# Performance work log

Measured on AMD Instinct MI355X. Metric: run time of the kernel, lower is better.

Reference implementation:

```python
import jax, jax.numpy as jnp
import numpy as np

B, S, D_IN, D_OUT, H = 4, 2048, 1024, 1024, 16
HD = D_OUT // H


def setup_inputs() -> dict:
    key = jax.random.key(0)
    ks = jax.random.split(key, 6)
    s_in = 1.0 / np.sqrt(D_IN)
    s_out = 1.0 / np.sqrt(D_OUT)
    return {
        "x": jax.random.normal(ks[0], (B, S, D_IN), dtype=jnp.float32),
        "W_q": jax.random.uniform(ks[1], (D_OUT, D_IN), jnp.float32, -s_in, s_in),
        "W_k": jax.random.uniform(ks[2], (D_OUT, D_IN), jnp.float32, -s_in, s_in),
        "W_v": jax.random.uniform(ks[3], (D_OUT, D_IN), jnp.float32, -s_in, s_in),
        "W_o": jax.random.uniform(ks[4], (D_OUT, D_OUT), jnp.float32, -s_out, s_out),
        "b_o": jax.random.uniform(ks[5], (D_OUT,), jnp.float32, -s_out, s_out),
    }


def reference(x, W_q, W_k, W_v, W_o, b_o):
    b, s, _ = x.shape
    # torch Linear: y = x @ W.T  (no qkv bias)
    q = (x @ W_q.T).reshape(b, s, H, HD).transpose(0, 2, 1, 3)  # [b,h,s,hd]
    k = (x @ W_k.T).reshape(b, s, H, HD).transpose(0, 2, 1, 3)
    v = (x @ W_v.T).reshape(b, s, H, HD).transpose(0, 2, 1, 3)
    scores = jnp.einsum("bhqd,bhkd->bhqk", q, k)  # [b,h,s,s]
    causal = jnp.triu(jnp.ones((s, s), dtype=bool), k=1)
    scores = jnp.where(causal, -jnp.inf, scores)
    attn = jax.nn.softmax(scores / np.sqrt(HD), axis=-1)
    # dropout p=0.0 -> identity
    ctx = jnp.einsum("bhqk,bhkd->bhqd", attn, v)  # [b,h,s,hd]
    ctx = ctx.transpose(0, 2, 1, 3).reshape(b, s, D_OUT)
    return ctx @ W_o.T + b_o
```

## Files before the change

kernel.cpp:

```cpp
#include <hip/hip_runtime.h>
#include <cstdint>
#include <cstddef>

#define S_LEN  2048
#define NHEAD  16
#define HDIM   64
#define KD     1024
#define BSROWS 8192

typedef __attribute__((ext_vector_type(4))) float          floatx4;
typedef __attribute__((ext_vector_type(8))) __bf16         bf16x8;
typedef __attribute__((ext_vector_type(8))) unsigned short ushort8v;
typedef __attribute__((ext_vector_type(4))) unsigned short ushort4v;
typedef __attribute__((ext_vector_type(4))) float          float4v;

__device__ __forceinline__ unsigned short f2bf(float f) {
  unsigned int u = __float_as_uint(f);
  u += 0x7fffu + ((u >> 16) & 1u);
  return (unsigned short)(u >> 16);
}

#if __has_builtin(__builtin_amdgcn_exp2f)
#define EXP2F(x) __builtin_amdgcn_exp2f(x)
#else
#define EXP2F(x) exp2f(x)
#endif

__device__ __forceinline__ unsigned int pack2bf(float a, float b) {
#if __has_builtin(__builtin_amdgcn_perm)
  return __builtin_amdgcn_perm(__float_as_uint(b), __float_as_uint(a), 0x07060302);
#else
  return (__float_as_uint(a) >> 16) | (__float_as_uint(b) & 0xffff0000u);
#endif
}

__device__ __forceinline__ void async_cp16(const void* gsrc, void* ldst) {
  __builtin_amdgcn_global_load_lds(
      (__attribute__((address_space(1))) void*)gsrc,
      (__attribute__((address_space(3))) void*)ldst,
      16, 0, 0);
}

#define XN4 2097152
#define WN4 262144

__global__ __launch_bounds__(256) void cvt_kernel(
    const float* __restrict__ x,  const float* __restrict__ wq,
    const float* __restrict__ wk, const float* __restrict__ wv,
    const float* __restrict__ wo,
    unsigned short* __restrict__ xb, unsigned short* __restrict__ wqkvb,
    unsigned short* __restrict__ wob)
{
  const int i = blockIdx.x * 256 + threadIdx.x;
  const float* src; unsigned short* dst; int off;
  if (i < XN4) { src = x; dst = xb; off = i; }
  else {
    const int j = i - XN4;
    if (j < WN4)          { src = wq; dst = wqkvb;           off = j; }
    else if (j < 2*WN4)   { src = wk; dst = wqkvb + 4*WN4;   off = j - WN4; }
    else if (j < 3*WN4)   { src = wv; dst = wqkvb + 8*WN4;   off = j - 2*WN4; }
    else                  { src = wo; dst = wob;             off = j - 3*WN4; }
  }
  const float4v v = ((const float4v*)src)[off];
  ushort4v o;
  o.x = f2bf(v.x); o.y = f2bf(v.y); o.z = f2bf(v.z); o.w = f2bf(v.w);
  ((ushort4v*)dst)[off] = o;
}

template<bool SWAP>
__device__ __forceinline__ void kloop128(
    const unsigned short* __restrict__ gA,
    const unsigned short* __restrict__ gB,
    unsigned short* smem, floatx4 (&acc)[4][4],
    const int wave, const int quad, const int l15,
    const int wr, const int wc)
{
  {
    unsigned short* lA = smem + wave * 1024;
    unsigned short* lB = smem + 4096 + wave * 1024;
    async_cp16(gA,                    lA);
    async_cp16(gA + (size_t)16 * KD,  lA + 512);
    async_cp16(gB,                    lB);
    async_cp16(gB + (size_t)16 * KD,  lB + 512);
  }
  const int lsw = (l15 >> 1) & 3;

#pragma unroll 2
  for (int it = 0; it < 32; it++) {
    asm volatile("s_waitcnt vmcnt(0) lgkmcnt(0)\n\ts_barrier" ::: "memory");
    if (it + 1 < 32) {
      const int nb = (it + 1) & 1;
      const int ko = (it + 1) * 32;
      unsigned short* lA = smem + nb * 8192 + wave * 1024;
      unsigned short* lB = smem + nb * 8192 + 4096 + wave * 1024;
      async_cp16(gA + ko,                   lA);
      async_cp16(gA + ko + (size_t)16 * KD, lA + 512);
      async_cp16(gB + ko,                   lB);
      async_cp16(gB + ko + (size_t)16 * KD, lB + 512);
    }
    const unsigned short* As = smem + (it & 1) * 8192;
    const unsigned short* Bs = As + 4096;

    bf16x8 af[4], bfrag[4];
#pragma unroll
    for (int i = 0; i < 4; i++)
      af[i] = *(const bf16x8*)&As[(wr * 64 + i * 16 + l15) * 32 + (quad ^ lsw) * 8];
#pragma unroll
    for (int j = 0; j < 4; j++)
      bfrag[j] = *(const bf16x8*)&Bs[(wc * 64 + j * 16 + l15) * 32 + (quad ^ lsw) * 8];
#pragma unroll
    for (int i = 0; i < 4; i++)
#pragma unroll
      for (int j = 0; j < 4; j++) {
        if (SWAP)
          acc[i][j] = __builtin_amdgcn_mfma_f32_16x16x32_bf16(bfrag[j], af[i], acc[i][j], 0, 0, 0);
        else
          acc[i][j] = __builtin_amdgcn_mfma_f32_16x16x32_bf16(af[i], bfrag[j], acc[i][j], 0, 0, 0);
      }
  }
}

__global__ __launch_bounds__(256) void gemm_qkv(
    const unsigned short* __restrict__ A,
    const unsigned short* __restrict__ Bw,
    unsigned short* __restrict__ Qo,
    unsigned short* __restrict__ Ko,
    unsigned short* __restrict__ Vto)
{
  __shared__ unsigned short smem[17408];
  const int tid  = threadIdx.x;
  const int wave = tid >> 6, lane = tid & 63;
  const int quad = lane >> 4, l15 = lane & 15;
  const int wr = wave >> 1, wc = wave & 1;
  const int m0 = blockIdx.x * 128, n0 = blockIdx.y * 128;

  const int srow = lane >> 2;
  const int scol = ((lane & 3) ^ ((srow >> 1) & 3)) * 8;
  const unsigned short* gA = A  + (size_t)(m0 + wave * 32 + srow) * KD + scol;
  const unsigned short* gB = Bw + (size_t)(n0 + wave * 32 + srow) * KD + scol;

  const floatx4 fzero = {0.f, 0.f, 0.f, 0.f};
  floatx4 acc[4][4];
#pragma unroll
  for (int i = 0; i < 4; i++)
#pragma unroll
    for (int j = 0; j < 4; j++) acc[i][j] = fzero;

  const int which = n0 >> 10;
  const int h0 = (n0 & 1023) >> 6;
  const int b = m0 >> 11, sl = m0 & 2047;

  if (which < 2) {
    kloop128<true>(gA, gB, smem, acc, wave, quad, l15, wr, wc);
    unsigned short* dst = which ? Ko : Qo;
    const float scale = which ? 1.0f : 0.18033688011112042f;
    __syncthreads();
    const int srw = wr * 64 + l15;
    const int scl = wc * 64 + quad * 4;
#pragma unroll
    for (int i = 0; i < 4; i++)
#pragma unroll
      for (int j = 0; j < 4; j++) {
        ushort4v t4;
#pragma unroll
        for (int r = 0; r < 4; r++) t4[r] = f2bf(acc[i][j][r] * scale);
        *(ushort4v*)&smem[(srw + i * 16) * 136 + scl + j * 16] = t4;
      }
    __syncthreads();
#pragma unroll
    for (int t = 0; t < 8; t++) {
      const int c   = t * 256 + tid;
      const int hd8 = (c & 7) * 8;
      const int hh  = (c >> 3) & 1;
      const int s   = c >> 4;
      const ushort8v val = *(const ushort8v*)&smem[s * 136 + hh * 64 + hd8];
      *(ushort8v*)&dst[((size_t)((b * NHEAD + h0 + hh) * S_LEN + sl + s)) * HDIM + hd8] = val;
    }
  } else {
    kloop128<false>(gA, gB, smem, acc, wave, quad, l15, wr, wc);
    __syncthreads();
    const int crow = wr * 64 + quad * 4;
    const int ccol = wc * 64 + l15;
#pragma unroll
    for (int i = 0; i < 4; i++)
#pragma unroll
      for (int j = 0; j < 4; j++) {
        ushort4v t4;
#pragma unroll
        for (int r = 0; r < 4; r++) t4[r] = f2bf(acc[i][j][r]);
        *(ushort4v*)&smem[(ccol + j * 16) * 136 + crow + i * 16] = t4;
      }
    __syncthreads();
#pragma unroll
    for (int t = 0; t < 8; t++) {
      const int c  = t * 256 + tid;
      const int nl = c >> 4, sc = (c & 15) * 8;
      const ushort8v val = *(const ushort8v*)&smem[nl * 136 + sc];
      *(ushort8v*)&Vto[((size_t)((b * NHEAD + h0 + (nl >> 6)) * HDIM + (nl & 63))) * S_LEN + sl + sc] = val;
    }
  }
}

__global__ __launch_bounds__(512, 6) void attn_kernel(
    const unsigned short* __restrict__ Qg_,
    const unsigned short* __restrict__ Kg_,
    const unsigned short* __restrict__ Vtg_,
    unsigned short* __restrict__ CTX)
{
  __shared__ unsigned short smem[25088];
  const int tid  = threadIdx.x, wave = tid >> 6, lane = tid & 63;
  const int quad = lane >> 4, l15 = lane & 15;
  unsigned short* Pw = smem + 16384 + wave * 1088;

  const int bh = (int)blockIdx.x;
  const int yy = (int)blockIdx.y;
  const int qt = (yy < 4) ? yy : (yy < 8) ? (11 - yy) : (yy < 12) ? yy : (27 - yy);
  const int q0 = qt * 128;
  const size_t base = (size_t)bh * (S_LEN * HDIM);
  const unsigned short* Qg  = Qg_  + base;
  const unsigned short* Kg  = Kg_  + base;
  const unsigned short* Vtg = Vtg_ + base;
  const int qw = q0 + wave * 16;

  const int strow = lane >> 3;
  const int stxc  = (lane & 7) ^ strow;
  const unsigned short* kstage = Kg  + (size_t)(wave * 8 + strow) * HDIM  + stxc * 8;
  const unsigned short* vstage = Vtg + (size_t)(wave * 8 + strow) * S_LEN + stxc * 8;
  unsigned short* kd0 = smem + wave * 512;
  unsigned short* vd0 = smem + 4096 + wave * 512;

  async_cp16(kstage, kd0);
  async_cp16(vstage, vd0);

  bf16x8 qf[2];
#pragma unroll
  for (int ks = 0; ks < 2; ks++)
    qf[ks] = *(const bf16x8*)&Qg[(size_t)(qw + l15) * HDIM + ks * 32 + quad * 8];

  const int sw0 = ((quad)     ^ (l15 & 7)) * 8;
  const int sw1 = ((4 + quad) ^ (l15 & 7)) * 8;

  const floatx4 fzero = {0.f, 0.f, 0.f, 0.f};
  floatx4 O[4];
  float l_part = 0.f;
#pragma unroll
  for (int mt = 0; mt < 4; mt++) O[mt] = fzero;

  const int ntiles = 2 * qt + 2;

  for (int j = 0; j < ntiles; j++) {
    asm volatile("s_waitcnt vmcnt(0) lgkmcnt(0)\n\ts_barrier" ::: "memory");
    if (j + 1 < ntiles) {
      const int nb = (j + 1) & 1;
      async_cp16(kstage + (size_t)(j + 1) * 64 * HDIM, kd0 + nb * 8192);
      async_cp16(vstage + (size_t)(j + 1) * 64,        vd0 + nb * 8192);
    }
    const int k0 = j * 64;
    if (k0 > qw + 15) continue;
    const unsigned short* Ksb = smem + (j & 1) * 8192;
    const unsigned short* Vsb = Ksb + 4096;
    const int krel = qw + 15 - k0;

    floatx4 sa[4];
#pragma unroll
    for (int kt = 0; kt < 4; kt++) sa[kt] = fzero;
    __builtin_amdgcn_s_setprio(1);
#pragma unroll
    for (int kt = 0; kt < 4; kt++) {
      if (kt * 16 <= krel) {
        const unsigned short* kr = &Ksb[(kt * 16 + l15) * 64];
        sa[kt] = __builtin_amdgcn_mfma_f32_16x16x32_bf16(*(const bf16x8*)(kr + sw0), qf[0], sa[kt], 0, 0, 0);
        sa[kt] = __builtin_amdgcn_mfma_f32_16x16x32_bf16(*(const bf16x8*)(kr + sw1), qf[1], sa[kt], 0, 0, 0);
      }
    }
    __builtin_amdgcn_s_setprio(0);

    const int qrow = qw + l15;
#pragma unroll
    for (int kt = 0; kt < 4; kt++) {
      const int kbase = k0 + kt * 16;
      unsigned short* pdst = &Pw[l15 * 68 + kt * 16 + quad * 4];
      if (kt * 16 <= krel) {
        if (kbase + 15 > qw) {
#pragma unroll
          for (int r = 0; r < 4; r++)
            if (kbase + quad * 4 + r > qrow) sa[kt][r] = -INFINITY;
        }
        const float p0 = EXP2F(sa[kt][0]), p1 = EXP2F(sa[kt][1]);
        const float p2 = EXP2F(sa[kt][2]), p3 = EXP2F(sa[kt][3]);
        l_part += (p0 + p1) + (p2 + p3);
        uint2 pk; pk.x = pack2bf(p0, p1); pk.y = pack2bf(p2, p3);
        *(uint2*)pdst = pk;
      } else if ((kt >> 1) * 32 <= krel) {
        uint2 z; z.x = 0u; z.y = 0u;
        *(uint2*)pdst = z;
      }
    }
    asm volatile("s_waitcnt lgkmcnt(0)" ::: "memory");

#pragma unroll
    for (int ks = 0; ks < 2; ks++) {
      if (ks * 32 > krel) break;
      const unsigned short* ps = &Pw[l15 * 68 + ks * 32 + quad * 8];
      union { ushort4v h[2]; bf16x8 v; } pu;
      pu.h[0] = *(const ushort4v*)ps;
      pu.h[1] = *(const ushort4v*)(ps + 4);
      __builtin_amdgcn_s_setprio(1);
#pragma unroll
      for (int mt = 0; mt < 4; mt++) {
        const bf16x8 vf = *(const bf16x8*)(&Vsb[(mt * 16 + l15) * 64] + (ks ? sw1 : sw0));
        O[mt] = __builtin_amdgcn_mfma_f32_16x16x32_bf16(vf, pu.v, O[mt], 0, 0, 0);
      }
      __builtin_amdgcn_s_setprio(0);
    }
  }

#pragma unroll
  for (int d = 16; d < 64; d <<= 1)
    l_part += __shfl_xor(l_part, d, 64);

  {
    const float inv = 1.0f / l_part;
#pragma unroll
    for (int mt = 0; mt < 4; mt++)
#pragma unroll
      for (int a = 0; a < 2; a++) {
        const unsigned int pk =
            (unsigned int)f2bf(O[mt][2 * a] * inv) |
            ((unsigned int)f2bf(O[mt][2 * a + 1] * inv) << 16);
        *(unsigned int*)&Pw[l15 * 68 + mt * 16 + quad * 4 + 2 * a] = pk;
      }
  }
  asm volatile("s_waitcnt lgkmcnt(0)" ::: "memory");
  const int b = bh >> 4, h = bh & 15;
#pragma unroll
  for (int it = 0; it < 2; it++) {
    const int g = it * 64 + lane;
    const int row = g >> 3, c8 = (g & 7) * 8;
    union { ushort4v h[2]; ushort8v v; } ou;
    ou.h[0] = *(const ushort4v*)&Pw[row * 68 + c8];
    ou.h[1] = *(const ushort4v*)&Pw[row * 68 + c8 + 4];
    const int s = qw + row;
    *(ushort8v*)&CTX[((size_t)(b * S_LEN + s)) * KD + h * HDIM + c8] = ou.v;
  }
}

__global__ __launch_bounds__(256) void gemm_out(
    const unsigned short* __restrict__ A,
    const unsigned short* __restrict__ Bw,
    const float* __restrict__ bias,
    float* __restrict__ out)
{
  __shared__ unsigned short smem[16384];
  const int tid  = threadIdx.x;
  const int wave = tid >> 6, lane = tid & 63;
  const int quad = lane >> 4, l15 = lane & 15;
  const int wr = wave >> 1, wc = wave & 1;
  const int m0 = blockIdx.x * 128, n0 = blockIdx.y * 128;

  const int srow = lane >> 2;
  const int scol = ((lane & 3) ^ ((srow >> 1) & 3)) * 8;
  const unsigned short* gA = A  + (size_t)(m0 + wave * 32 + srow) * KD + scol;
  const unsigned short* gB = Bw + (size_t)(n0 + wave * 32 + srow) * KD + scol;

  const floatx4 fzero = {0.f, 0.f, 0.f, 0.f};
  floatx4 acc[4][4];
#pragma unroll
  for (int i = 0; i < 4; i++)
#pragma unroll
    for (int j = 0; j < 4; j++) acc[i][j] = fzero;

  kloop128<true>(gA, gB, smem, acc, wave, quad, l15, wr, wc);

#pragma unroll
  for (int j = 0; j < 4; j++) {
    const int nb4 = n0 + wc * 64 + j * 16 + quad * 4;
    const float4v bb = *(const float4v*)&bias[nb4];
#pragma unroll
    for (int i = 0; i < 4; i++) {
      const int m = m0 + wr * 64 + i * 16 + l15;
      float4v st;
#pragma unroll
      for (int r = 0; r < 4; r++) st[r] = acc[i][j][r] + bb[r];
      *(float4v*)&out[(size_t)m * KD + nb4] = st;
    }
  }
}

extern "C" void kernel_launch(void* const* d_in, const int* in_sizes, int n_in,
                              void* d_out, int out_size, void* d_ws, size_t ws_size,
                              hipStream_t stream) {
  (void)in_sizes; (void)n_in; (void)out_size;
  const float* x  = (const float*)d_in[0];
  const float* wq = (const float*)d_in[1];
  const float* wk = (const float*)d_in[2];
  const float* wv = (const float*)d_in[3];
  const float* wo = (const float*)d_in[4];
  const float* bo = (const float*)d_in[5];
  float* out = (float*)d_out;

  if (ws_size < (size_t)92274688) return;
  char* ws = (char*)d_ws;
  unsigned short* xb    = (unsigned short*)(ws);
  unsigned short* wqkvb = (unsigned short*)(ws + (size_t)16777216);
  unsigned short* wob   = (unsigned short*)(ws + (size_t)23068672);
  unsigned short* qws   = (unsigned short*)(ws + (size_t)25165824);
  unsigned short* kws   = (unsigned short*)(ws + (size_t)41943040);
  unsigned short* vtws  = (unsigned short*)(ws + (size_t)58720256);
  unsigned short* ctxws = (unsigned short*)(ws + (size_t)75497472);

  cvt_kernel<<<12288, 256, 0, stream>>>(x, wq, wk, wv, wo, xb, wqkvb, wob);
  gemm_qkv<<<dim3(64, 24), 256, 0, stream>>>(xb, wqkvb, qws, kws, vtws);
  attn_kernel<<<dim3(64, 16), 512, 0, stream>>>(qws, kws, vtws, ctxws);
  gemm_out<<<dim3(64, 8), 256, 0, stream>>>(ctxws, wob, bo, out);
}
```

Measured before the change: 242.5 us.

## Replace QKV GEMM with 256x256-tile, 8-wave, double-buffered pipelined kernel

Swaps the 128x128 QKV projection GEMM for a 256x256-tile kernel with 512 threads. It uses a 64-wide K step, double-buffered async global-to-LDS staging interleaved with MFMA quarter-blocks, s_setprio around the MFMAs, and a remapped block order for L2 locality. The aim is more data reuse per LDS load and better overlap of memory with compute. In exchange it uses a 128KB LDS footprint, more accumulator registers and fewer blocks (384), which risks occupancy and tail effects.

```diff
diff --git a/kernel.cpp b/kernel.cpp
--- a/kernel.cpp
+++ b/kernel.cpp
@@ -65,6 +65,188 @@
   ushort4v o;
   o.x = f2bf(v.x); o.y = f2bf(v.y); o.z = f2bf(v.z); o.w = f2bf(v.w);
   ((ushort4v*)dst)[off] = o;
+}
+
+__device__ __forceinline__ void stage_j(
+    int j, const unsigned short* __restrict__ gAs,
+    const unsigned short* __restrict__ gBs,
+    unsigned short* smem, const int wave)
+{
+  const int tk  = j >> 2, pos = j & 3;
+  const int bufo = (tk & 1) << 15;
+  const bool isA = (pos == 0) | (pos == 3);
+  const int rowbase = (pos >= 2) ? 128 : 0;
+  const unsigned short* g = (isA ? gAs : gBs) + (size_t)rowbase * KD + tk * 64;
+  unsigned short* l = smem + bufo + (isA ? 0 : 16384) + rowbase * 64 + wave * 512;
+  async_cp16(g,                  l);
+  async_cp16(g + (size_t)64 * KD, l + 4096);
+}
+
+template<bool SWAP>
+__device__ __forceinline__ void kloop256(
+    const unsigned short* __restrict__ gAs,
+    const unsigned short* __restrict__ gBs,
+    unsigned short* smem, floatx4 (&acc)[8][4],
+    const int wave, const int quad, const int l15)
+{
+  const int ar_base = (wave >> 2) * 64 + l15;
+  const int br_base = (wave & 3) * 32 + l15;
+  const int sw0 = ((quad)     ^ (l15 & 7)) * 8;
+  const int sw1 = ((4 + quad) ^ (l15 & 7)) * 8;
+
+  bf16x8 af[4][2];
+  bf16x8 bfr[2][2][2];
+
+#pragma unroll
+  for (int j = 0; j < 6; ++j) stage_j(j, gAs, gBs, smem, wave);
+
+#define LOADA(mh)                                                              \
+  _Pragma("unroll") for (int mt = 0; mt < 4; ++mt) {                           \
+    const unsigned short* ar = &As[((mh) * 128 + ar_base + mt * 16) * 64];     \
+    af[mt][0] = *(const bf16x8*)(ar + sw0);                                    \
+    af[mt][1] = *(const bf16x8*)(ar + sw1);                                    \
+  }
+#define LOADB(nh)                                                              \
+  _Pragma("unroll") for (int nt = 0; nt < 2; ++nt) {                           \
+    const unsigned short* br = &Bs[((nh) * 128 + br_base + nt * 16) * 64];     \
+    bfr[nh][nt][0] = *(const bf16x8*)(br + sw0);                               \
+    bfr[nh][nt][1] = *(const bf16x8*)(br + sw1);                               \
+  }
+#define MFMAQ(mh, nh)                                                          \
+  __builtin_amdgcn_s_setprio(1);                                               \
+  _Pragma("unroll") for (int mt = 0; mt < 4; ++mt)                             \
+    _Pragma("unroll") for (int nt = 0; nt < 2; ++nt)                           \
+      _Pragma("unroll") for (int ks = 0; ks < 2; ++ks) {                       \
+        if (SWAP)                                                              \
+          acc[(mh)*4+mt][(nh)*2+nt] = __builtin_amdgcn_mfma_f32_16x16x32_bf16( \
+              bfr[nh][nt][ks], af[mt][ks], acc[(mh)*4+mt][(nh)*2+nt], 0,0,0);  \
+        else                                                                   \
+          acc[(mh)*4+mt][(nh)*2+nt] = __builtin_amdgcn_mfma_f32_16x16x32_bf16( \
+              af[mt][ks], bfr[nh][nt][ks], acc[(mh)*4+mt][(nh)*2+nt], 0,0,0);  \
+      }                                                                        \
+  __builtin_amdgcn_s_setprio(0);
+
+#pragma unroll 2
+  for (int t = 0; t < 16; ++t) {
+    const unsigned short* As = smem + ((t & 1) << 15);
+    const unsigned short* Bs = As + 16384;
+    const int j0 = 4 * t + 6;
+
+    asm volatile("s_barrier" ::: "memory");
+    if (j0 < 64) stage_j(j0, gAs, gBs, smem, wave);
+    if (t < 15) asm volatile("s_waitcnt vmcnt(6)\n\ts_barrier" ::: "memory");
+    else        asm volatile("s_waitcnt vmcnt(0)\n\ts_barrier" ::: "memory");
+    LOADA(0)
+    LOADB(0)
+    MFMAQ(0, 0)
+
+    asm volatile("s_barrier" ::: "memory");
+    if (j0 + 1 < 64) stage_j(j0 + 1, gAs, gBs, smem, wave);
+    LOADB(1)
+    MFMAQ(0, 1)
+
+    asm volatile("s_barrier" ::: "memory");
+    if (j0 + 2 < 64) stage_j(j0 + 2, gAs, gBs, smem, wave);
+    LOADA(1)
+    MFMAQ(1, 0)
+
+    asm volatile("s_barrier" ::: "memory");
+    if (j0 + 3 < 64) stage_j(j0 + 3, gAs, gBs, smem, wave);
+    MFMAQ(1, 1)
+  }
+#undef LOADA
+#undef LOADB
+#undef MFMAQ
+}
+
+__global__ __launch_bounds__(512, 2) void gemm_qkv8(
+    const unsigned short* __restrict__ A,
+    const unsigned short* __restrict__ Bw,
+    unsigned short* __restrict__ Qo,
+    unsigned short* __restrict__ Ko,
+    unsigned short* __restrict__ Vto)
+{
+  __shared__ unsigned short smem[65536];
+  const int tid  = threadIdx.x;
+  const int wave = tid >> 6, lane = tid & 63;
+  const int quad = lane >> 4, l15 = lane & 15;
+
+  const int bid = (int)blockIdx.x;
+  const int tau = (bid & 7) * 48 + (bid >> 3);
+  const int m0 = (tau / 12) * 256, n0 = (tau % 12) * 256;
+
+  const int strow = tid >> 3;
+  const int stxc  = (tid & 7) ^ (strow & 7);
+  const unsigned short* gAs = A  + (size_t)(m0 + strow) * KD + stxc * 8;
+  const unsigned short* gBs = Bw + (size_t)(n0 + strow) * KD + stxc * 8;
+
+  const floatx4 fzero = {0.f, 0.f, 0.f, 0.f};
+  floatx4 acc[8][4];
+#pragma unroll
+  for (int i = 0; i < 8; i++)
+#pragma unroll
+    for (int j = 0; j < 4; j++) acc[i][j] = fzero;
+
+  const int which = n0 >> 10;
+  if (which < 2) kloop256<true >(gAs, gBs, smem, acc, wave, quad, l15);
+  else           kloop256<false>(gAs, gBs, smem, acc, wave, quad, l15);
+
+  const int h0 = (n0 & 1023) >> 6;
+  const int b = m0 >> 11, sl = m0 & 2047;
+  __syncthreads();
+
+  if (which < 2) {
+    unsigned short* dst = which ? Ko : Qo;
+    const float scale = which ? 1.0f : 0.18033688011112042f;
+#pragma unroll
+    for (int mh = 0; mh < 2; ++mh) {
+      if (mh) __syncthreads();
+#pragma unroll
+      for (int mt = 0; mt < 4; ++mt)
+#pragma unroll
+        for (int jn = 0; jn < 4; ++jn) {
+          ushort4v t4;
+#pragma unroll
+          for (int r = 0; r < 4; ++r) t4[r] = f2bf(acc[mh * 4 + mt][jn][r] * scale);
+          const int row = (wave >> 2) * 64 + mt * 16 + l15;
+          const int col = (jn >> 1) * 128 + (wave & 3) * 32 + (jn & 1) * 16 + quad * 4;
+          *(ushort4v*)&smem[row * 264 + col] = t4;
+        }
+      __syncthreads();
+#pragma unroll
+      for (int t8 = 0; t8 < 8; ++t8) {
+        const int c = t8 * 512 + tid;
+        const int sr = c >> 5, ch = c & 31;
+        const int hs = ch >> 3, hd8 = (ch & 7) * 8;
+        const ushort8v val = *(const ushort8v*)&smem[sr * 264 + hs * 64 + hd8];
+        *(ushort8v*)&dst[((size_t)((b * NHEAD + h0 + hs) * S_LEN + sl + mh * 128 + sr)) * HDIM + hd8] = val;
+      }
+    }
+  } else {
+#pragma unroll
+    for (int mh = 0; mh < 2; ++mh) {
+      if (mh) __syncthreads();
+#pragma unroll
+      for (int mt = 0; mt < 4; ++mt)
+#pragma unroll
+        for (int jn = 0; jn < 4; ++jn) {
+          ushort4v t4;
+#pragma unroll
+          for (int r = 0; r < 4; ++r) t4[r] = f2bf(acc[mh * 4 + mt][jn][r]);
+          const int nl = (jn >> 1) * 128 + (wave & 3) * 32 + (jn & 1) * 16 + l15;
+          const int sc = (wave >> 2) * 64 + mt * 16 + quad * 4;
+          *(ushort4v*)&smem[nl * 136 + sc] = t4;
+        }
+      __syncthreads();
+#pragma unroll
+      for (int t8 = 0; t8 < 8; ++t8) {
+        const int c = t8 * 512 + tid;
+        const int nl = c >> 4, sc = (c & 15) * 8;
+        const ushort8v val = *(const ushort8v*)&smem[nl * 136 + sc];
+        *(ushort8v*)&Vto[((size_t)((b * NHEAD + h0 + (nl >> 6)) * HDIM + (nl & 63))) * S_LEN + sl + mh * 128 + sc] = val;
+      }
+    }
+  }
 }
 
 template<bool SWAP>
@@ -120,87 +302,6 @@
   }
 }
 
-__global__ __launch_bounds__(256) void gemm_qkv(
-    const unsigned short* __restrict__ A,
-    const unsigned short* __restrict__ Bw,
-    unsigned short* __restrict__ Qo,
-    unsigned short* __restrict__ Ko,
-    unsigned short* __restrict__ Vto)
-{
-  __shared__ unsigned short smem[17408];
-  const int tid  = threadIdx.x;
-  const int wave = tid >> 6, lane = tid & 63;
-  const int quad = lane >> 4, l15 = lane & 15;
-  const int wr = wave >> 1, wc = wave & 1;
-  const int m0 = blockIdx.x * 128, n0 = blockIdx.y * 128;
-
-  const int srow = lane >> 2;
-  const int scol = ((lane & 3) ^ ((srow >> 1) & 3)) * 8;
-  const unsigned short* gA = A  + (size_t)(m0 + wave * 32 + srow) * KD + scol;
-  const unsigned short* gB = Bw + (size_t)(n0 + wave * 32 + srow) * KD + scol;
-
-  const floatx4 fzero = {0.f, 0.f, 0.f, 0.f};
-  floatx4 acc[4][4];
-#pragma unroll
-  for (int i = 0; i < 4; i++)
-#pragma unroll
-    for (int j = 0; j < 4; j++) acc[i][j] = fzero;
-
-  const int which = n0 >> 10;
-  const int h0 = (n0 & 1023) >> 6;
-  const int b = m0 >> 11, sl = m0 & 2047;
-
-  if (which < 2) {
-    kloop128<true>(gA, gB, smem, acc, wave, quad, l15, wr, wc);
-    unsigned short* dst = which ? Ko : Qo;
-    const float scale = which ? 1.0f : 0.18033688011112042f;
-    __syncthreads();
-    const int srw = wr * 64 + l15;
-    const int scl = wc * 64 + quad * 4;
-#pragma unroll
-    for (int i = 0; i < 4; i++)
-#pragma unroll
-      for (int j = 0; j < 4; j++) {
-        ushort4v t4;
-#pragma unroll
-        for (int r = 0; r < 4; r++) t4[r] = f2bf(acc[i][j][r] * scale);
-        *(ushort4v*)&smem[(srw + i * 16) * 136 + scl + j * 16] = t4;
-      }
-    __syncthreads();
-#pragma unroll
-    for (int t = 0; t < 8; t++) {
-      const int c   = t * 256 + tid;
-      const int hd8 = (c & 7) * 8;
-      const int hh  = (c >> 3) & 1;
-      const int s   = c >> 4;
-      const ushort8v val = *(const ushort8v*)&smem[s * 136 + hh * 64 + hd8];
-      *(ushort8v*)&dst[((size_t)((b * NHEAD + h0 + hh) * S_LEN + sl + s)) * HDIM + hd8] = val;
-    }
-  } else {
-    kloop128<false>(gA, gB, smem, acc, wave, quad, l15, wr, wc);
-    __syncthreads();
-    const int crow = wr * 64 + quad * 4;
-    const int ccol = wc * 64 + l15;
-#pragma unroll
-    for (int i = 0; i < 4; i++)
-#pragma unroll
-      for (int j = 0; j < 4; j++) {
-        ushort4v t4;
-#pragma unroll
-        for (int r = 0; r < 4; r++) t4[r] = f2bf(acc[i][j][r]);
-        *(ushort4v*)&smem[(ccol + j * 16) * 136 + crow + i * 16] = t4;
-      }
-    __syncthreads();
-#pragma unroll
-    for (int t = 0; t < 8; t++) {
-      const int c  = t * 256 + tid;
-      const int nl = c >> 4, sc = (c & 15) * 8;
-      const ushort8v val = *(const ushort8v*)&smem[nl * 136 + sc];
-      *(ushort8v*)&Vto[((size_t)((b * NHEAD + h0 + (nl >> 6)) * HDIM + (nl & 63))) * S_LEN + sl + sc] = val;
-    }
-  }
-}
-
 __global__ __launch_bounds__(512, 6) void attn_kernel(
     const unsigned short* __restrict__ Qg_,
     const unsigned short* __restrict__ Kg_,
@@ -410,7 +511,7 @@
   unsigned short* ctxws = (unsigned short*)(ws + (size_t)75497472);
 
   cvt_kernel<<<12288, 256, 0, stream>>>(x, wq, wk, wv, wo, xb, wqkvb, wob);
-  gemm_qkv<<<dim3(64, 24), 256, 0, stream>>>(xb, wqkvb, qws, kws, vtws);
+  gemm_qkv8<<<384, 512, 0, stream>>>(xb, wqkvb, qws, kws, vtws);
   attn_kernel<<<dim3(64, 16), 512, 0, stream>>>(qws, kws, vtws, ctxws);
   gemm_out<<<dim3(64, 8), 256, 0, stream>>>(ctxws, wob, bo, out);
 }
```

Measured after the change: 230.3 us. 5.0% less time.
